# Performance work log

Hardware: AMD Instinct MI355X
Metric: run time of the kernel (lower is better)

Reference implementation:

```python
import jax, jax.numpy as jnp
import numpy as np

E = 1024
H = 16
HD = E // H  # 64


def setup_inputs() -> dict:
    key = jax.random.key(0)
    ks = jax.random.split(key, 5)
    x = jax.random.normal(ks[0], (2, 2048, E), dtype=jnp.float32)
    s = 1.0 / np.sqrt(E)
    W_qkv = jax.random.uniform(ks[1], (E, 3 * E), jnp.float32, -s, s)
    b_qkv = jax.random.uniform(ks[2], (3 * E,), jnp.float32, -s, s)
    W_out = jax.random.uniform(ks[3], (E, E), jnp.float32, -s, s)
    b_out = jax.random.uniform(ks[4], (E,), jnp.float32, -s, s)
    return {"x": x, "W_qkv": W_qkv, "b_qkv": b_qkv, "W_out": W_out, "b_out": b_out}


def reference(x, W_qkv, b_qkv, W_out, b_out):
    B, N, _ = x.shape
    scale = HD ** (-0.5)
    qkv = x @ W_qkv + b_qkv                         # [B, N, 3E]
    qkv = qkv.reshape(B, N, H, 3 * HD)              # torch layout: per-head 3*hd chunk
    qkv = qkv.transpose(0, 2, 1, 3)                 # [B, H, N, 3*hd]
    q, k, v = jnp.split(qkv, 3, axis=-1)            # each [B, H, N, hd]
    attn = jnp.einsum('bhqd,bhkd->bhqk', q, k) * scale
    attn = jax.nn.softmax(attn, axis=-1)            # dropout is identity in eval
    out = jnp.einsum('bhqk,bhkd->bhqd', attn, v)    # [B, H, N, hd]
    out = out.transpose(0, 2, 1, 3).reshape(B, N, E)
    return out @ W_out + b_out
```

## Files before the change

### kernel.cpp

```cpp
#include <hip/hip_runtime.h>


#define SEQ 2048
#define NH  16

typedef __attribute__((ext_vector_type(8))) short short8;
typedef __attribute__((ext_vector_type(4))) short short4v;
typedef __attribute__((ext_vector_type(4))) float floatx4;
typedef __attribute__((ext_vector_type(4))) _Float16 half4;
typedef __attribute__((ext_vector_type(8))) _Float16 half8;
typedef __attribute__((ext_vector_type(2))) _Float16 half2v;
typedef __attribute__((ext_vector_type(2))) __fp16 fp16x2;

#define QSCALE 0.1803368801111204f

__device__ __forceinline__ short f2bf(float f) {
    union { float f; unsigned u; } v; v.f = f;
    unsigned r = v.u + 0x7fffu + ((v.u >> 16) & 1u);
    return (short)(r >> 16);
}

__device__ __forceinline__ float fast_exp2(float x) {
#if __has_builtin(__builtin_amdgcn_exp2f)
    return __builtin_amdgcn_exp2f(x);
#else
    return exp2f(x);
#endif
}

__device__ __forceinline__ half2v cvt_pk(float a, float b) {
#if __has_builtin(__builtin_amdgcn_cvt_pkrtz)
    union { fp16x2 i; half2v o; } u;
    u.i = __builtin_amdgcn_cvt_pkrtz(a, b);
    return u.o;
#else
    half2v r; r.x = (_Float16)a; r.y = (_Float16)b; return r;
#endif
}

#define GLDS16(gp, lp)                                                          \
    __builtin_amdgcn_global_load_lds(                                           \
        (const __attribute__((address_space(1))) unsigned int*)(gp),            \
        (__attribute__((address_space(3))) unsigned int*)(lp), 16, 0, 0)

__global__ __launch_bounds__(256) void prep_kernel(
    const float* __restrict__ x,  short* __restrict__ xb,
    const float* __restrict__ wq, short* __restrict__ wqkvt,
    const float* __restrict__ wo, short* __restrict__ woutt)
{
    const int tid = threadIdx.x;
    const int b = blockIdx.x;
    if (b < 2048) {
        int i = b * 256 + tid;
        const float4* in4 = (const float4*)x + (size_t)i * 2;
        float4 a = in4[0], c = in4[1];
        short8 o = { f2bf(a.x), f2bf(a.y), f2bf(a.z), f2bf(a.w),
                     f2bf(c.x), f2bf(c.y), f2bf(c.z), f2bf(c.w) };
        *((short8*)xb + i) = o;
        return;
    }
    __shared__ float T[64][65];
    const float* in; short* out; int R, C, c0, r0;
    if (b < 2816) {
        int t = b - 2048; in = wq; out = wqkvt; R = 1024; C = 3072;
        c0 = (t % 48) * 64; r0 = (t / 48) * 64;
    } else {
        int t = b - 2816; in = wo; out = woutt; R = 1024; C = 1024;
        c0 = (t & 15) * 64; r0 = (t >> 4) * 64;
    }
#pragma unroll
    for (int it = 0; it < 4; ++it) {
        int r = it * 16 + (tid >> 4), c = (tid & 15) * 4;
        float4 v = *(const float4*)(in + (size_t)(r0 + r) * C + c0 + c);
        T[c+0][r] = v.x; T[c+1][r] = v.y; T[c+2][r] = v.z; T[c+3][r] = v.w;
    }
    __syncthreads();
#pragma unroll
    for (int it = 0; it < 4; ++it) {
        int oc = it * 16 + (tid >> 4), k = (tid & 15) * 4;
        short4v o = { f2bf(T[oc][k]), f2bf(T[oc][k+1]), f2bf(T[oc][k+2]), f2bf(T[oc][k+3]) };
        *(short4v*)(out + (size_t)(c0 + oc) * R + r0 + k) = o;
    }
}

#define GEMM_CORE(A_PTR, B_PTR, LDA, LDB)                                        \
    __shared__ short As[128 * 32];                                               \
    __shared__ short Bs[128 * 32];                                               \
    const int tid  = threadIdx.x;                                                \
    const int lane = tid & 63, w = tid >> 6;                                     \
    const int quad = lane >> 4, l16 = lane & 15;                                 \
    const int wm = w >> 1, wn = w & 1;                                           \
    const int c0 = blockIdx.x * 128, r0 = blockIdx.y * 128;                      \
    floatx4 acc[4][4];                                                           \
    _Pragma("unroll")                                                            \
    for (int i = 0; i < 4; ++i)                                                  \
        _Pragma("unroll")                                                        \
        for (int j = 0; j < 4; ++j) acc[i][j] = (floatx4){0.f, 0.f, 0.f, 0.f};   \
    const int srow = tid >> 2;                                                   \
    const int sgx  = ((tid & 3) ^ ((srow >> 1) & 3)) * 8;                        \
    const short* Ag = (A_PTR) + (size_t)(r0 + srow) * (LDA) + sgx;               \
    const short* Bg = (B_PTR) + (size_t)(c0 + srow) * (LDB) + sgx;               \
    const int fsw = (l16 >> 1) & 3;                                              \
    for (int kk = 0; kk < 1024; kk += 32) {                                      \
        __syncthreads();                                                         \
        GLDS16(Ag + kk,                      As + tid * 8);                      \
        GLDS16(Ag + (size_t)64 * (LDA) + kk, As + 2048 + tid * 8);               \
        GLDS16(Bg + kk,                      Bs + tid * 8);                      \
        GLDS16(Bg + (size_t)64 * (LDB) + kk, Bs + 2048 + tid * 8);               \
        __syncthreads();                                                         \
        short8 af[4], bf[4];                                                     \
        _Pragma("unroll")                                                        \
        for (int mt = 0; mt < 4; ++mt)                                           \
            af[mt] = *(const short8*)&As[(wm * 64 + mt * 16 + l16) * 32 + (quad ^ fsw) * 8]; \
        _Pragma("unroll")                                                        \
        for (int nt = 0; nt < 4; ++nt)                                           \
            bf[nt] = *(const short8*)&Bs[(wn * 64 + nt * 16 + l16) * 32 + (quad ^ fsw) * 8]; \
        _Pragma("unroll")                                                        \
        for (int mt = 0; mt < 4; ++mt)                                           \
            _Pragma("unroll")                                                    \
            for (int nt = 0; nt < 4; ++nt)                                       \
                acc[mt][nt] = __builtin_amdgcn_mfma_f32_16x16x32_bf16(           \
                    af[mt], bf[nt], acc[mt][nt], 0, 0, 0);                       \
    }

__global__ __launch_bounds__(256) void qkv_gemm_kernel(
    const short* __restrict__ wt, const short* __restrict__ xb,
    const float* __restrict__ bias,
    short* __restrict__ qb, short* __restrict__ kb, _Float16* __restrict__ vfb)
{
    GEMM_CORE(wt, xb, 1024, 1024)
#pragma unroll
    for (int mt = 0; mt < 4; ++mt) {
        int oc0 = r0 + wm * 64 + mt * 16 + quad * 4;
        int head = oc0 / 192;
        int t = (oc0 - head * 192) >> 6;
        int d0 = oc0 & 63;
        float4 bv = *(const float4*)(bias + oc0);
#pragma unroll
        for (int nt = 0; nt < 4; ++nt) {
            int tok = c0 + wn * 64 + nt * 16 + l16;
            int bh = (tok >> 11) * NH + head;
            float v0 = acc[mt][nt][0] + bv.x, v1 = acc[mt][nt][1] + bv.y;
            float v2 = acc[mt][nt][2] + bv.z, v3 = acc[mt][nt][3] + bv.w;
            if (t == 2) {
                int n  = tok & (SEQ - 1);
                int h  = nt & 1;
                int qv = l16 >> 2, r = l16 & 3;
                int j  = h * 4 + r;
                size_t vb = (size_t)bh * 131072 + (size_t)(n >> 7) * 8192
                          + (size_t)((n >> 5) & 3) * 2048 + (size_t)d0 * 32 + j;
                _Float16 vv[4] = { (_Float16)v0, (_Float16)v1,
                                   (_Float16)v2, (_Float16)v3 };
#pragma unroll
                for (int jj = 0; jj < 4; ++jj) {
                    int cset = qv ^ (((d0 + jj) >> 1) & 3);
                    vfb[vb + jj * 32 + cset * 8] = vv[jj];
                }
            } else {
                size_t base = ((size_t)bh * SEQ + (tok & (SEQ - 1))) * 64 + d0;
                if (t == 0) {
                    short4v o = { f2bf(v0 * QSCALE), f2bf(v1 * QSCALE),
                                  f2bf(v2 * QSCALE), f2bf(v3 * QSCALE) };
                    *(short4v*)(qb + base) = o;
                } else {
                    short4v o = { f2bf(v0), f2bf(v1), f2bf(v2), f2bf(v3) };
                    *(short4v*)(kb + base) = o;
                }
            }
        }
    }
}

__global__ __launch_bounds__(256) void out_gemm_kernel(
    const short* __restrict__ wt, const short* __restrict__ ab,
    const float* __restrict__ bias, float* __restrict__ out)
{
    __shared__ short As[64 * 32];
    __shared__ short Bs[128 * 32];
    const int tid  = threadIdx.x;
    const int lane = tid & 63, w = tid >> 6;
    const int quad = lane >> 4, l16 = lane & 15;
    const int c0 = blockIdx.x * 128;
    const int r0 = blockIdx.y * 64;
    floatx4 acc[4][2];
#pragma unroll
    for (int i = 0; i < 4; ++i)
#pragma unroll
        for (int j = 0; j < 2; ++j) acc[i][j] = (floatx4){0.f, 0.f, 0.f, 0.f};
    const int srow = tid >> 2;
    const int sgx  = ((tid & 3) ^ ((srow >> 1) & 3)) * 8;
    const short* Ag = wt + (size_t)(r0 + srow) * 1024 + sgx;
    const short* Bg = ab + (size_t)(c0 + srow) * 1024 + sgx;
    const int fsw = (l16 >> 1) & 3;
    for (int kk = 0; kk < 1024; kk += 32) {
        __syncthreads();
        GLDS16(Ag + kk,                   As + tid * 8);
        GLDS16(Bg + kk,                   Bs + tid * 8);
        GLDS16(Bg + (size_t)64 * 1024 + kk, Bs + 2048 + tid * 8);
        __syncthreads();
        short8 af[4], bf[2];
#pragma unroll
        for (int mt = 0; mt < 4; ++mt)
            af[mt] = *(const short8*)&As[(mt * 16 + l16) * 32 + (quad ^ fsw) * 8];
#pragma unroll
        for (int nt = 0; nt < 2; ++nt)
            bf[nt] = *(const short8*)&Bs[(w * 32 + nt * 16 + l16) * 32 + (quad ^ fsw) * 8];
#pragma unroll
        for (int mt = 0; mt < 4; ++mt)
#pragma unroll
            for (int nt = 0; nt < 2; ++nt)
                acc[mt][nt] = __builtin_amdgcn_mfma_f32_16x16x32_bf16(
                    af[mt], bf[nt], acc[mt][nt], 0, 0, 0);
    }
#pragma unroll
    for (int mt = 0; mt < 4; ++mt) {
        int oc0 = r0 + mt * 16 + quad * 4;
        float4 bv = *(const float4*)(bias + oc0);
#pragma unroll
        for (int nt = 0; nt < 2; ++nt) {
            int tok = c0 + w * 32 + nt * 16 + l16;
            float4 o = { acc[mt][nt][0] + bv.x, acc[mt][nt][1] + bv.y,
                         acc[mt][nt][2] + bv.z, acc[mt][nt][3] + bv.w };
            *(float4*)(out + (size_t)tok * 1024 + oc0) = o;
        }
    }
}

__global__ __launch_bounds__(256, 2) void attn_kernel(
    const short* __restrict__ qb, const short* __restrict__ kb,
    const _Float16* __restrict__ vfb, short* __restrict__ ob)
{
    __shared__ short    Ks[2][128 * 64];
    __shared__ _Float16 Vts[2][64 * 128];
    const int tid  = threadIdx.x;
    const int lane = tid & 63, w = tid >> 6;
    const int quad = lane >> 4, l16 = lane & 15;
    const int lb = blockIdx.x;
    const int bh = (lb & 7) + (((lb >> 3) & 3) << 3);
    const int q0 = (lb >> 5) * 128;

    short8 aq[2][2];
#pragma unroll
    for (int qf = 0; qf < 2; ++qf) {
        const short* qp = qb + ((size_t)bh * SEQ + q0 + w * 32 + qf * 16 + l16) * 64 + quad * 8;
        aq[qf][0] = *(const short8*)(qp);
        aq[qf][1] = *(const short8*)(qp + 32);
    }

    const int krow = tid >> 3, kg = tid & 7;
    const short* kgp = kb + ((size_t)bh * SEQ + krow) * 64 + (kg ^ (krow & 7)) * 8;
    const short* vgp = (const short*)(vfb + (size_t)bh * 131072) + tid * 8;

    floatx4 o_acc[4][2];
#pragma unroll
    for (int dt = 0; dt < 4; ++dt)
#pragma unroll
        for (int qf = 0; qf < 2; ++qf) o_acc[dt][qf] = (floatx4){0.f, 0.f, 0.f, 0.f};
    float lw[2] = {0.f, 0.f};

    {
        GLDS16(kgp,        &Ks[0][0] + tid * 8);
        GLDS16(kgp + 2048, &Ks[0][0] + 2048 + tid * 8);
        GLDS16(kgp + 4096, &Ks[0][0] + 4096 + tid * 8);
        GLDS16(kgp + 6144, &Ks[0][0] + 6144 + tid * 8);
        GLDS16(vgp,        (short*)&Vts[0][0] + tid * 8);
        GLDS16(vgp + 2048, (short*)&Vts[0][0] + 2048 + tid * 8);
        GLDS16(vgp + 4096, (short*)&Vts[0][0] + 4096 + tid * 8);
        GLDS16(vgp + 6144, (short*)&Vts[0][0] + 6144 + tid * 8);
    }
    __syncthreads();

    int cur = 0;
    for (int k0 = 0; k0 < SEQ; k0 += 128) {
        if (k0 + 128 < SEQ) {
            const short* kn = kgp + (size_t)(k0 + 128) * 64;
            short* kd = &Ks[cur ^ 1][0];
            GLDS16(kn,        kd + tid * 8);
            GLDS16(kn + 2048, kd + 2048 + tid * 8);
            GLDS16(kn + 4096, kd + 4096 + tid * 8);
            GLDS16(kn + 6144, kd + 6144 + tid * 8);
            const short* vn = vgp + (size_t)(k0 + 128) * 64;
            short* vd = (short*)&Vts[cur ^ 1][0];
            GLDS16(vn,        vd + tid * 8);
            GLDS16(vn + 2048, vd + 2048 + tid * 8);
            GLDS16(vn + 4096, vd + 4096 + tid * 8);
            GLDS16(vn + 6144, vd + 6144 + tid * 8);
        }

        const short* ksc = &Ks[cur][0];
        const short* vsc = (const short*)&Vts[cur][0];
#pragma unroll
        for (int u = 0; u < 4; ++u) {
            half8 av8[4];
#pragma unroll
            for (int dt = 0; dt < 4; ++dt) {
                union { short8 s; half8 h; } vv;
                vv.s = *(const short8*)(vsc + u * 2048
                        + (dt * 16 + l16) * 32 + (quad ^ ((l16 >> 1) & 3)) * 8);
                av8[dt] = vv.h;
            }
            floatx4 sacc[2][2];
#pragma unroll
            for (int h = 0; h < 2; ++h) {
                const short* krp = ksc + (u * 32 + h * 16 + l16) * 64;
                short8 ak0 = *(const short8*)(krp + ((0 + quad) ^ (l16 & 7)) * 8);
                short8 ak1 = *(const short8*)(krp + ((4 + quad) ^ (l16 & 7)) * 8);
                __builtin_amdgcn_s_setprio(1);
#pragma unroll
                for (int qf = 0; qf < 2; ++qf) {
                    floatx4 z = (floatx4){0.f, 0.f, 0.f, 0.f};
                    z = __builtin_amdgcn_mfma_f32_16x16x32_bf16(ak0, aq[qf][0], z, 0, 0, 0);
                    sacc[h][qf] = __builtin_amdgcn_mfma_f32_16x16x32_bf16(ak1, aq[qf][1], z, 0, 0, 0);
                }
                __builtin_amdgcn_s_setprio(0);
            }
            half8 pf8[2];
#pragma unroll
            for (int qf = 0; qf < 2; ++qf) {
                float p0 = fast_exp2(sacc[0][qf][0]);
                float p1 = fast_exp2(sacc[0][qf][1]);
                float p2 = fast_exp2(sacc[0][qf][2]);
                float p3 = fast_exp2(sacc[0][qf][3]);
                float p4 = fast_exp2(sacc[1][qf][0]);
                float p5 = fast_exp2(sacc[1][qf][1]);
                float p6 = fast_exp2(sacc[1][qf][2]);
                float p7 = fast_exp2(sacc[1][qf][3]);
                lw[qf] += ((p0 + p1) + (p2 + p3)) + ((p4 + p5) + (p6 + p7));
                half2v a = cvt_pk(p0, p1), b = cvt_pk(p2, p3);
                half2v c = cvt_pk(p4, p5), d = cvt_pk(p6, p7);
                pf8[qf] = (half8){a.x, a.y, b.x, b.y, c.x, c.y, d.x, d.y};
            }
            __builtin_amdgcn_s_setprio(1);
#pragma unroll
            for (int dt = 0; dt < 4; ++dt)
#pragma unroll
                for (int qf = 0; qf < 2; ++qf)
                    o_acc[dt][qf] = __builtin_amdgcn_mfma_f32_16x16x32_f16(
                        av8[dt], pf8[qf], o_acc[dt][qf], 0, 0, 0);
            __builtin_amdgcn_s_setprio(0);
        }

        __syncthreads();
        cur ^= 1;
    }

    float inv[2];
#pragma unroll
    for (int qf = 0; qf < 2; ++qf) {
        lw[qf] += __shfl_xor(lw[qf], 16);
        lw[qf] += __shfl_xor(lw[qf], 32);
        inv[qf] = 1.0f / lw[qf];
    }

    const int b = bh >> 4, h = bh & 15;
#pragma unroll
    for (int dt = 0; dt < 4; ++dt)
#pragma unroll
        for (int qf = 0; qf < 2; ++qf) {
            int tok = b * SEQ + q0 + w * 32 + qf * 16 + l16;
            floatx4 o = o_acc[dt][qf];
            short4v o4 = { f2bf(o[0] * inv[qf]), f2bf(o[1] * inv[qf]),
                           f2bf(o[2] * inv[qf]), f2bf(o[3] * inv[qf]) };
            *(short4v*)(ob + (size_t)tok * 1024 + h * 64 + dt * 16 + quad * 4) = o4;
        }
}

extern "C" void kernel_launch(void* const* d_in, const int* in_sizes, int n_in,
                              void* d_out, int out_size, void* d_ws, size_t ws_size,
                              hipStream_t stream) {
    const float* x     = (const float*)d_in[0];
    const float* W_qkv = (const float*)d_in[1];
    const float* b_qkv = (const float*)d_in[2];
    const float* W_out = (const float*)d_in[3];
    const float* b_out = (const float*)d_in[4];
    float* out = (float*)d_out;

    short* xb      = (short*)d_ws;
    short* wqkvt   = xb    + (size_t)4096 * 1024;
    short* woutt   = wqkvt + (size_t)3072 * 1024;
    short* qb      = woutt + (size_t)1024 * 1024;
    short* kb      = qb    + (size_t)32 * SEQ * 64;
    _Float16* vfb  = (_Float16*)(kb + (size_t)32 * SEQ * 64);
    short* ob      = (short*)(vfb + (size_t)32 * 64 * SEQ);

    prep_kernel<<<3072, 256, 0, stream>>>(x, xb, W_qkv, wqkvt, W_out, woutt);
    qkv_gemm_kernel<<<dim3(32, 24), 256, 0, stream>>>(wqkvt, xb, b_qkv, qb, kb, vfb);
    attn_kernel<<<512, 256, 0, stream>>>(qb, kb, vfb, ob);
    out_gemm_kernel<<<dim3(32, 16), 256, 0, stream>>>(woutt, ob, b_out, out);
}
```

Baseline: 174.0 us.

## Double-buffer LDS tiles in QKV and output GEMM main loops

Both GEMM kernels now keep two LDS buffers per operand. Each iteration issues the global-to-LDS loads for the next K tile before the MFMA work on the current one, so fetch latency can overlap compute and only one barrier is needed per iteration. The cost is doubled LDS use per block, which may lower occupancy. Whether the direct-to-LDS loads are really waited on before the single barrier depends on how GLDS16 and the compiler insert vmcnt waits.

```diff
diff --git a/kernel.cpp b/kernel.cpp
--- a/kernel.cpp
+++ b/kernel.cpp
@@ -83,9 +83,9 @@
     }
 }
 
-#define GEMM_CORE(A_PTR, B_PTR, LDA, LDB)                                        \
-    __shared__ short As[128 * 32];                                               \
-    __shared__ short Bs[128 * 32];                                               \
+#define GEMM_CORE_DB(A_PTR, B_PTR, LDA, LDB)                                     \
+    __shared__ short As[2][128 * 32];                                            \
+    __shared__ short Bs[2][128 * 32];                                            \
     const int tid  = threadIdx.x;                                                \
     const int lane = tid & 63, w = tid >> 6;                                     \
     const int quad = lane >> 4, l16 = lane & 15;                                 \
@@ -101,26 +101,34 @@
     const short* Ag = (A_PTR) + (size_t)(r0 + srow) * (LDA) + sgx;               \
     const short* Bg = (B_PTR) + (size_t)(c0 + srow) * (LDB) + sgx;               \
     const int fsw = (l16 >> 1) & 3;                                              \
+    GLDS16(Ag,                      &As[0][0] + tid * 8);                        \
+    GLDS16(Ag + (size_t)64 * (LDA), &As[0][0] + 2048 + tid * 8);                 \
+    GLDS16(Bg,                      &Bs[0][0] + tid * 8);                        \
+    GLDS16(Bg + (size_t)64 * (LDB), &Bs[0][0] + 2048 + tid * 8);                 \
+    __syncthreads();                                                             \
+    int cur = 0;                                                                 \
     for (int kk = 0; kk < 1024; kk += 32) {                                      \
-        __syncthreads();                                                         \
-        GLDS16(Ag + kk,                      As + tid * 8);                      \
-        GLDS16(Ag + (size_t)64 * (LDA) + kk, As + 2048 + tid * 8);               \
-        GLDS16(Bg + kk,                      Bs + tid * 8);                      \
-        GLDS16(Bg + (size_t)64 * (LDB) + kk, Bs + 2048 + tid * 8);               \
-        __syncthreads();                                                         \
+        if (kk + 32 < 1024) {                                                    \
+            GLDS16(Ag + kk + 32,                      &As[cur ^ 1][0] + tid * 8);        \
+            GLDS16(Ag + (size_t)64 * (LDA) + kk + 32, &As[cur ^ 1][0] + 2048 + tid * 8); \
+            GLDS16(Bg + kk + 32,                      &Bs[cur ^ 1][0] + tid * 8);        \
+            GLDS16(Bg + (size_t)64 * (LDB) + kk + 32, &Bs[cur ^ 1][0] + 2048 + tid * 8); \
+        }                                                                        \
         short8 af[4], bf[4];                                                     \
         _Pragma("unroll")                                                        \
         for (int mt = 0; mt < 4; ++mt)                                           \
-            af[mt] = *(const short8*)&As[(wm * 64 + mt * 16 + l16) * 32 + (quad ^ fsw) * 8]; \
+            af[mt] = *(const short8*)&As[cur][(wm * 64 + mt * 16 + l16) * 32 + (quad ^ fsw) * 8]; \
         _Pragma("unroll")                                                        \
         for (int nt = 0; nt < 4; ++nt)                                           \
-            bf[nt] = *(const short8*)&Bs[(wn * 64 + nt * 16 + l16) * 32 + (quad ^ fsw) * 8]; \
+            bf[nt] = *(const short8*)&Bs[cur][(wn * 64 + nt * 16 + l16) * 32 + (quad ^ fsw) * 8]; \
         _Pragma("unroll")                                                        \
         for (int mt = 0; mt < 4; ++mt)                                           \
             _Pragma("unroll")                                                    \
             for (int nt = 0; nt < 4; ++nt)                                       \
                 acc[mt][nt] = __builtin_amdgcn_mfma_f32_16x16x32_bf16(           \
                     af[mt], bf[nt], acc[mt][nt], 0, 0, 0);                       \
+        __syncthreads();                                                         \
+        cur ^= 1;                                                                \
     }
 
 __global__ __launch_bounds__(256) void qkv_gemm_kernel(
@@ -128,7 +136,7 @@
     const float* __restrict__ bias,
     short* __restrict__ qb, short* __restrict__ kb, _Float16* __restrict__ vfb)
 {
-    GEMM_CORE(wt, xb, 1024, 1024)
+    GEMM_CORE_DB(wt, xb, 1024, 1024)
 #pragma unroll
     for (int mt = 0; mt < 4; ++mt) {
         int oc0 = r0 + wm * 64 + mt * 16 + quad * 4;
@@ -175,8 +183,8 @@
     const short* __restrict__ wt, const short* __restrict__ ab,
     const float* __restrict__ bias, float* __restrict__ out)
 {
-    __shared__ short As[64 * 32];
-    __shared__ short Bs[128 * 32];
+    __shared__ short As[2][64 * 32];
+    __shared__ short Bs[2][128 * 32];
     const int tid  = threadIdx.x;
     const int lane = tid & 63, w = tid >> 6;
     const int quad = lane >> 4, l16 = lane & 15;
@@ -192,25 +200,32 @@
     const short* Ag = wt + (size_t)(r0 + srow) * 1024 + sgx;
     const short* Bg = ab + (size_t)(c0 + srow) * 1024 + sgx;
     const int fsw = (l16 >> 1) & 3;
+    GLDS16(Ag,                      &As[0][0] + tid * 8);
+    GLDS16(Bg,                      &Bs[0][0] + tid * 8);
+    GLDS16(Bg + (size_t)64 * 1024,  &Bs[0][0] + 2048 + tid * 8);
+    __syncthreads();
+    int cur = 0;
     for (int kk = 0; kk < 1024; kk += 32) {
-        __syncthreads();
-        GLDS16(Ag + kk,                   As + tid * 8);
-        GLDS16(Bg + kk,                   Bs + tid * 8);
-        GLDS16(Bg + (size_t)64 * 1024 + kk, Bs + 2048 + tid * 8);
-        __syncthreads();
+        if (kk + 32 < 1024) {
+            GLDS16(Ag + kk + 32,                     &As[cur ^ 1][0] + tid * 8);
+            GLDS16(Bg + kk + 32,                     &Bs[cur ^ 1][0] + tid * 8);
+            GLDS16(Bg + (size_t)64 * 1024 + kk + 32, &Bs[cur ^ 1][0] + 2048 + tid * 8);
+        }
         short8 af[4], bf[2];
 #pragma unroll
         for (int mt = 0; mt < 4; ++mt)
-            af[mt] = *(const short8*)&As[(mt * 16 + l16) * 32 + (quad ^ fsw) * 8];
+            af[mt] = *(const short8*)&As[cur][(mt * 16 + l16) * 32 + (quad ^ fsw) * 8];
 #pragma unroll
         for (int nt = 0; nt < 2; ++nt)
-            bf[nt] = *(const short8*)&Bs[(w * 32 + nt * 16 + l16) * 32 + (quad ^ fsw) * 8];
+            bf[nt] = *(const short8*)&Bs[cur][(w * 32 + nt * 16 + l16) * 32 + (quad ^ fsw) * 8];
 #pragma unroll
         for (int mt = 0; mt < 4; ++mt)
 #pragma unroll
             for (int nt = 0; nt < 2; ++nt)
                 acc[mt][nt] = __builtin_amdgcn_mfma_f32_16x16x32_bf16(
                     af[mt], bf[nt], acc[mt][nt], 0, 0, 0);
+        __syncthreads();
+        cur ^= 1;
     }
 #pragma unroll
     for (int mt = 0; mt < 4; ++mt) {
```

Result: slower. 180.0 us (+3.4%).

## Use 8 waves per attention block, 16 query rows per wave

Applied to the files above, without the earlier changes.

The attention kernel now runs 512 threads per block with each wave handling 16 query rows instead of 32. Each thread loads half as many K/V tile chunks, so per-wave registers shrink and more waves can be resident to hide latency. In exchange, each K/V fragment read from LDS feeds fewer MFMAs, which doubles LDS read traffic per unit of compute. Launch bounds move to (512,4), which may constrain register allocation.

```diff
diff --git a/kernel.cpp b/kernel.cpp
--- a/kernel.cpp
+++ b/kernel.cpp
@@ -226,7 +226,7 @@
     }
 }
 
-__global__ __launch_bounds__(256, 2) void attn_kernel(
+__global__ __launch_bounds__(512, 4) void attn_kernel(
     const short* __restrict__ qb, const short* __restrict__ kb,
     const _Float16* __restrict__ vfb, short* __restrict__ ob)
 {
@@ -239,34 +239,27 @@
     const int bh = (lb & 7) + (((lb >> 3) & 3) << 3);
     const int q0 = (lb >> 5) * 128;
 
-    short8 aq[2][2];
-#pragma unroll
-    for (int qf = 0; qf < 2; ++qf) {
-        const short* qp = qb + ((size_t)bh * SEQ + q0 + w * 32 + qf * 16 + l16) * 64 + quad * 8;
-        aq[qf][0] = *(const short8*)(qp);
-        aq[qf][1] = *(const short8*)(qp + 32);
+    short8 aq0, aq1;
+    {
+        const short* qp = qb + ((size_t)bh * SEQ + q0 + w * 16 + l16) * 64 + quad * 8;
+        aq0 = *(const short8*)(qp);
+        aq1 = *(const short8*)(qp + 32);
     }
 
     const int krow = tid >> 3, kg = tid & 7;
     const short* kgp = kb + ((size_t)bh * SEQ + krow) * 64 + (kg ^ (krow & 7)) * 8;
     const short* vgp = (const short*)(vfb + (size_t)bh * 131072) + tid * 8;
 
-    floatx4 o_acc[4][2];
-#pragma unroll
-    for (int dt = 0; dt < 4; ++dt)
-#pragma unroll
-        for (int qf = 0; qf < 2; ++qf) o_acc[dt][qf] = (floatx4){0.f, 0.f, 0.f, 0.f};
-    float lw[2] = {0.f, 0.f};
+    floatx4 o_acc[4];
+#pragma unroll
+    for (int dt = 0; dt < 4; ++dt) o_acc[dt] = (floatx4){0.f, 0.f, 0.f, 0.f};
+    float lw = 0.f;
 
     {
-        GLDS16(kgp,        &Ks[0][0] + tid * 8);
-        GLDS16(kgp + 2048, &Ks[0][0] + 2048 + tid * 8);
-        GLDS16(kgp + 4096, &Ks[0][0] + 4096 + tid * 8);
-        GLDS16(kgp + 6144, &Ks[0][0] + 6144 + tid * 8);
-        GLDS16(vgp,        (short*)&Vts[0][0] + tid * 8);
-        GLDS16(vgp + 2048, (short*)&Vts[0][0] + 2048 + tid * 8);
-        GLDS16(vgp + 4096, (short*)&Vts[0][0] + 4096 + tid * 8);
-        GLDS16(vgp + 6144, (short*)&Vts[0][0] + 6144 + tid * 8);
+        GLDS16(kgp,                      &Ks[0][0] + tid * 8);
+        GLDS16(kgp + (size_t)64 * 64,    &Ks[0][0] + 4096 + tid * 8);
+        GLDS16(vgp,                      (short*)&Vts[0][0] + tid * 8);
+        GLDS16(vgp + 4096,               (short*)&Vts[0][0] + 4096 + tid * 8);
     }
     __syncthreads();
 
@@ -275,16 +268,12 @@
         if (k0 + 128 < SEQ) {
             const short* kn = kgp + (size_t)(k0 + 128) * 64;
             short* kd = &Ks[cur ^ 1][0];
-            GLDS16(kn,        kd + tid * 8);
-            GLDS16(kn + 2048, kd + 2048 + tid * 8);
-            GLDS16(kn + 4096, kd + 4096 + tid * 8);
-            GLDS16(kn + 6144, kd + 6144 + tid * 8);
+            GLDS16(kn,                    kd + tid * 8);
+            GLDS16(kn + (size_t)64 * 64,  kd + 4096 + tid * 8);
             const short* vn = vgp + (size_t)(k0 + 128) * 64;
             short* vd = (short*)&Vts[cur ^ 1][0];
-            GLDS16(vn,        vd + tid * 8);
-            GLDS16(vn + 2048, vd + 2048 + tid * 8);
-            GLDS16(vn + 4096, vd + 4096 + tid * 8);
-            GLDS16(vn + 6144, vd + 6144 + tid * 8);
+            GLDS16(vn,                    vd + tid * 8);
+            GLDS16(vn + 4096,             vd + 4096 + tid * 8);
         }
 
         const short* ksc = &Ks[cur][0];
@@ -299,44 +288,35 @@
                         + (dt * 16 + l16) * 32 + (quad ^ ((l16 >> 1) & 3)) * 8);
                 av8[dt] = vv.h;
             }
-            floatx4 sacc[2][2];
+            floatx4 sacc[2];
 #pragma unroll
             for (int h = 0; h < 2; ++h) {
                 const short* krp = ksc + (u * 32 + h * 16 + l16) * 64;
                 short8 ak0 = *(const short8*)(krp + ((0 + quad) ^ (l16 & 7)) * 8);
                 short8 ak1 = *(const short8*)(krp + ((4 + quad) ^ (l16 & 7)) * 8);
                 __builtin_amdgcn_s_setprio(1);
-#pragma unroll
-                for (int qf = 0; qf < 2; ++qf) {
-                    floatx4 z = (floatx4){0.f, 0.f, 0.f, 0.f};
-                    z = __builtin_amdgcn_mfma_f32_16x16x32_bf16(ak0, aq[qf][0], z, 0, 0, 0);
-                    sacc[h][qf] = __builtin_amdgcn_mfma_f32_16x16x32_bf16(ak1, aq[qf][1], z, 0, 0, 0);
-                }
+                floatx4 z = (floatx4){0.f, 0.f, 0.f, 0.f};
+                z = __builtin_amdgcn_mfma_f32_16x16x32_bf16(ak0, aq0, z, 0, 0, 0);
+                sacc[h] = __builtin_amdgcn_mfma_f32_16x16x32_bf16(ak1, aq1, z, 0, 0, 0);
                 __builtin_amdgcn_s_setprio(0);
             }
-            half8 pf8[2];
-#pragma unroll
-            for (int qf = 0; qf < 2; ++qf) {
-                float p0 = fast_exp2(sacc[0][qf][0]);
-                float p1 = fast_exp2(sacc[0][qf][1]);
-                float p2 = fast_exp2(sacc[0][qf][2]);
-                float p3 = fast_exp2(sacc[0][qf][3]);
-                float p4 = fast_exp2(sacc[1][qf][0]);
-                float p5 = fast_exp2(sacc[1][qf][1]);
-                float p6 = fast_exp2(sacc[1][qf][2]);
-                float p7 = fast_exp2(sacc[1][qf][3]);
-                lw[qf] += ((p0 + p1) + (p2 + p3)) + ((p4 + p5) + (p6 + p7));
-                half2v a = cvt_pk(p0, p1), b = cvt_pk(p2, p3);
-                half2v c = cvt_pk(p4, p5), d = cvt_pk(p6, p7);
-                pf8[qf] = (half8){a.x, a.y, b.x, b.y, c.x, c.y, d.x, d.y};
-            }
+            float p0 = fast_exp2(sacc[0][0]);
+            float p1 = fast_exp2(sacc[0][1]);
+            float p2 = fast_exp2(sacc[0][2]);
+            float p3 = fast_exp2(sacc[0][3]);
+            float p4 = fast_exp2(sacc[1][0]);
+            float p5 = fast_exp2(sacc[1][1]);
+            float p6 = fast_exp2(sacc[1][2]);
+            float p7 = fast_exp2(sacc[1][3]);
+            lw += ((p0 + p1) + (p2 + p3)) + ((p4 + p5) + (p6 + p7));
+            half2v a = cvt_pk(p0, p1), b = cvt_pk(p2, p3);
+            half2v c = cvt_pk(p4, p5), d = cvt_pk(p6, p7);
+            half8 pf8 = (half8){a.x, a.y, b.x, b.y, c.x, c.y, d.x, d.y};
             __builtin_amdgcn_s_setprio(1);
 #pragma unroll
             for (int dt = 0; dt < 4; ++dt)
-#pragma unroll
-                for (int qf = 0; qf < 2; ++qf)
-                    o_acc[dt][qf] = __builtin_amdgcn_mfma_f32_16x16x32_f16(
-                        av8[dt], pf8[qf], o_acc[dt][qf], 0, 0, 0);
+                o_acc[dt] = __builtin_amdgcn_mfma_f32_16x16x32_f16(
+                    av8[dt], pf8, o_acc[dt], 0, 0, 0);
             __builtin_amdgcn_s_setprio(0);
         }
 
@@ -344,25 +324,19 @@
         cur ^= 1;
     }
 
-    float inv[2];
-#pragma unroll
-    for (int qf = 0; qf < 2; ++qf) {
-        lw[qf] += __shfl_xor(lw[qf], 16);
-        lw[qf] += __shfl_xor(lw[qf], 32);
-        inv[qf] = 1.0f / lw[qf];
-    }
+    lw += __shfl_xor(lw, 16);
+    lw += __shfl_xor(lw, 32);
+    const float inv = 1.0f / lw;
 
     const int b = bh >> 4, h = bh & 15;
-#pragma unroll
-    for (int dt = 0; dt < 4; ++dt)
-#pragma unroll
-        for (int qf = 0; qf < 2; ++qf) {
-            int tok = b * SEQ + q0 + w * 32 + qf * 16 + l16;
-            floatx4 o = o_acc[dt][qf];
-            short4v o4 = { f2bf(o[0] * inv[qf]), f2bf(o[1] * inv[qf]),
-                           f2bf(o[2] * inv[qf]), f2bf(o[3] * inv[qf]) };
-            *(short4v*)(ob + (size_t)tok * 1024 + h * 64 + dt * 16 + quad * 4) = o4;
-        }
+    const int tok = b * SEQ + q0 + w * 16 + l16;
+#pragma unroll
+    for (int dt = 0; dt < 4; ++dt) {
+        floatx4 o = o_acc[dt];
+        short4v o4 = { f2bf(o[0] * inv), f2bf(o[1] * inv),
+                       f2bf(o[2] * inv), f2bf(o[3] * inv) };
+        *(short4v*)(ob + (size_t)tok * 1024 + h * 64 + dt * 16 + quad * 4) = o4;
+    }
 }
 
 extern "C" void kernel_launch(void* const* d_in, const int* in_sizes, int n_in,
@@ -385,6 +359,6 @@
 
     prep_kernel<<<3072, 256, 0, stream>>>(x, xb, W_qkv, wqkvt, W_out, woutt);
     qkv_gemm_kernel<<<dim3(32, 24), 256, 0, stream>>>(wqkvt, xb, b_qkv, qb, kb, vfb);
-    attn_kernel<<<512, 256, 0, stream>>>(qb, kb, vfb, ob);
+    attn_kernel<<<512, 512, 0, stream>>>(qb, kb, vfb, ob);
     out_gemm_kernel<<<dim3(32, 16), 256, 0, stream>>>(woutt, ob, b_out, out);
 }
```

Result: no change. 174.1 us (+0.0%).
